# Optimization experiments

Measured on AMD Instinct MI355X. Metric: run time of the kernel, lower is better.

## Reference

```python
import jax, jax.numpy as jnp
import numpy as np

B, S, E, H = 2, 2048, 2048, 16
D = E // H  # head_dim = 128


def _rope_tables(seq_len, dim):
    # standard RoPE: theta_i = 10000^(-2i/dim), angles duplicated over pair halves
    inv_freq = 1.0 / (10000.0 ** (np.arange(0, dim, 2, dtype=np.float32) / dim))
    angles = np.arange(seq_len, dtype=np.float32)[:, None] * inv_freq[None, :]  # [S, D/2]
    angles = np.concatenate([angles, angles], axis=-1)  # [S, D]
    return jnp.asarray(np.cos(angles)), jnp.asarray(np.sin(angles))


def setup_inputs() -> dict:
    key = jax.random.key(0)
    ks = jax.random.split(key, 10)
    sc = 1.0 / np.sqrt(E)
    cos, sin = _rope_tables(S, D)
    mask = jnp.tril(jnp.ones((S, S), dtype=bool))[None, None]  # causal [1,1,S,S]
    return {
        "x_q": jax.random.normal(ks[0], (B, S, E), jnp.float32),
        "x_kv": jax.random.normal(ks[1], (B, S, E), jnp.float32),
        "cos": cos,
        "sin": sin,
        "wq": jax.random.normal(ks[2], (E, E), jnp.float32) * sc,
        "bq": jax.random.normal(ks[3], (E,), jnp.float32) * 0.01,
        "wk": jax.random.normal(ks[4], (E, E), jnp.float32) * sc,
        "bk": jax.random.normal(ks[5], (E,), jnp.float32) * 0.01,
        "wv": jax.random.normal(ks[6], (E, E), jnp.float32) * sc,
        "bv": jax.random.normal(ks[7], (E,), jnp.float32) * 0.01,
        "wo": jax.random.normal(ks[8], (E, E), jnp.float32) * sc,
        "bo": jax.random.normal(ks[9], (E,), jnp.float32) * 0.01,
        "mask": mask,
    }


def _apply_rope(x, cos, sin):
    # x: [B,H,S,D]; cos/sin: [S,D]. rotate-half convention.
    x1, x2 = jnp.split(x, 2, axis=-1)
    rot = jnp.concatenate([-x2, x1], axis=-1)
    return x * cos[None, None] + rot * sin[None, None]


def reference(x_q, x_kv, cos, sin, wq, bq, wk, bk, wv, bv, wo, bo, mask):
    b, sq, _ = x_q.shape
    skv = x_kv.shape[1]
    q = (x_q @ wq.T + bq).reshape(b, sq, H, D).transpose(0, 2, 1, 3)   # [B,H,Sq,D]
    k = (x_kv @ wk.T + bk).reshape(b, skv, H, D).transpose(0, 2, 1, 3)
    v = (x_kv @ wv.T + bv).reshape(b, skv, H, D).transpose(0, 2, 1, 3)
    q = _apply_rope(q, cos, sin)
    k = _apply_rope(k, cos, sin)
    scores = jnp.einsum("bhqd,bhkd->bhqk", q, k) / jnp.sqrt(jnp.float32(D))
    scores = jnp.where(mask, scores, jnp.float32(-1e9))
    w = jax.nn.softmax(scores, axis=-1)  # dropout p=0 -> identity
    out = jnp.einsum("bhqk,bhkd->bhqd", w, v)
    out = out.transpose(0, 2, 1, 3).reshape(b, sq, H * D)
    return out @ wo.T + bo
```

## Files before the change

### kernel.cpp

```cpp
#include <hip/hip_runtime.h>
#include <hip/hip_bf16.h>

#define Bb 2
#define Ss 2048
#define Ee 2048
#define Hh 16
#define Dd 128
#define Mrows (Bb*Ss)

typedef short short8 __attribute__((ext_vector_type(8)));
typedef float f32x4 __attribute__((ext_vector_type(4)));

__device__ __forceinline__ unsigned short bf_rne(float f) {
    unsigned u = __builtin_bit_cast(unsigned, f);
    u += 0x7fffu + ((u >> 16) & 1u);
    return (unsigned short)(u >> 16);
}
__device__ __forceinline__ float bf2f(unsigned short x) {
    unsigned u = ((unsigned)x) << 16;
    return __builtin_bit_cast(float, u);
}
__device__ __forceinline__ void load_lds16(const void* g, void* l) {
    __builtin_amdgcn_global_load_lds(
        (const __attribute__((address_space(1))) unsigned int*)g,
        (__attribute__((address_space(3))) unsigned int*)l, 16, 0, 0);
}

__global__ void cast4_kernel(const float4* __restrict__ in, ushort4* __restrict__ out, int n4) {
    int i = blockIdx.x * 256 + threadIdx.x;
    if (i < n4) {
        float4 v = in[i];
        ushort4 o;
        o.x = bf_rne(v.x); o.y = bf_rne(v.y); o.z = bf_rne(v.z); o.w = bf_rne(v.w);
        out[i] = o;
    }
}

__global__ __launch_bounds__(256) void gemm_bt(
    const short* __restrict__ A, const short* __restrict__ W,
    const float* __restrict__ bias, float* __restrict__ Cf, short* __restrict__ Cb,
    int M, int N, int K, int mode)
{
    __shared__ short As[128*32];
    __shared__ short Bs[128*32];
    const int tid  = threadIdx.x;
    const int wave = tid >> 6;
    const int lane = tid & 63;
    const int quad = lane >> 4;
    const int l16  = lane & 15;
    const int m0 = blockIdx.x * 128;
    const int n0 = blockIdx.y * 128;
    const int wm = (wave & 1) * 64;
    const int wn = (wave >> 1) * 64;

    f32x4 acc[4][4] = {};

    const int srow = wave * 32 + (lane >> 2);
    const int scol = (lane & 3) * 8;
    const size_t a_base = (size_t)(m0 + srow) * K + scol;
    const size_t b_base = (size_t)(n0 + srow) * K + scol;

    for (int kt = 0; kt < K; kt += 32) {
        __syncthreads();
        load_lds16(A + a_base + kt,                 &As[(wave*32) * 32]);
        load_lds16(A + a_base + (size_t)16*K + kt,  &As[(wave*32 + 16) * 32]);
        load_lds16(W + b_base + kt,                 &Bs[(wave*32) * 32]);
        load_lds16(W + b_base + (size_t)16*K + kt,  &Bs[(wave*32 + 16) * 32]);
        __syncthreads();

        short8 af[4], bfr[4];
        #pragma unroll
        for (int i = 0; i < 4; ++i)
            af[i] = *(const short8*)&As[(wm + i*16 + l16)*32 + quad*8];
        #pragma unroll
        for (int j = 0; j < 4; ++j)
            bfr[j] = *(const short8*)&Bs[(wn + j*16 + l16)*32 + quad*8];
        #pragma unroll
        for (int i = 0; i < 4; ++i)
            #pragma unroll
            for (int j = 0; j < 4; ++j)
                acc[i][j] = __builtin_amdgcn_mfma_f32_16x16x32_bf16(af[i], bfr[j], acc[i][j], 0, 0, 0);
    }

    #pragma unroll
    for (int i = 0; i < 4; ++i) {
        #pragma unroll
        for (int j = 0; j < 4; ++j) {
            #pragma unroll
            for (int r = 0; r < 4; ++r) {
                int gm = m0 + wm + i*16 + quad*4 + r;
                int gn = n0 + wn + j*16 + l16;
                if (mode == 0) {
                    Cf[(size_t)gm * N + gn] = acc[i][j][r] + bias[gn];
                } else if (mode == 1) {
                    float v = acc[i][j][r] + bias[gn];
                    int b = gm >> 11, s = gm & (Ss-1);
                    int h = gn >> 7,  d = gn & (Dd-1);
                    Cb[(((size_t)(b*Hh + h)) * Ss + s) * Dd + d] = (short)bf_rne(v);
                } else {
                    float v = acc[i][j][r] + bias[gm];
                    int h = gm >> 7,  d = gm & (Dd-1);
                    int b = gn >> 11, s = gn & (Ss-1);
                    Cb[(((size_t)(b*Hh + h)) * Dd + d) * Ss + s] = (short)bf_rne(v);
                }
            }
        }
    }
}

__global__ void rope_kernel(short* __restrict__ X, const float* __restrict__ cosT,
                            const float* __restrict__ sinT, float scale) {
    int idx = blockIdx.x * 256 + threadIdx.x;
    int d  = idx & 63;
    int s  = (idx >> 6) & (Ss - 1);
    int bh = idx >> 17;
    size_t base = ((size_t)bh * Ss + s) * Dd;
    float x1 = bf2f((unsigned short)X[base + d]);
    float x2 = bf2f((unsigned short)X[base + d + 64]);
    float c  = cosT[s*Dd + d];
    float sn = sinT[s*Dd + d];
    float y1 = (x1 * c - x2 * sn) * scale;
    float y2 = (x2 * c + x1 * sn) * scale;
    X[base + d]      = (short)bf_rne(y1);
    X[base + d + 64] = (short)bf_rne(y2);
}

__global__ __launch_bounds__(256, 2) void attn_kernel(
    const short* __restrict__ Q, const short* __restrict__ Kk,
    const short* __restrict__ VT, short* __restrict__ O)
{
    __shared__ short Ks[64*128];
    __shared__ short Vt[2][128*64];
    __shared__ short Pw[4][32*72];

    const int tid  = threadIdx.x;
    const int wave = tid >> 6;
    const int lane = tid & 63;
    const int quad = lane >> 4;
    const int l16  = lane & 15;
    const int mmap = (blockIdx.x + blockIdx.y) & 15;
    const int qt   = (blockIdx.y & 16) ? (15 - mmap) : mmap;
    const int bh = blockIdx.y;
    const int b  = bh >> 4, h = bh & 15;
    const size_t head_off = (size_t)bh * Ss * Dd;
    const short* Kg  = Kk + head_off;
    const short* VTg = VT + head_off;

    auto stageK = [&](int kt) {
        #pragma unroll
        for (int j = 0; j < 4; ++j) {
            int r = wave*16 + j*4 + (lane >> 4);
            int c = (lane & 15) ^ (r & 15);
            load_lds16(Kg + (size_t)(kt*64 + r)*Dd + c*8, &Ks[(wave*16 + j*4)*128]);
        }
    };
    auto stageV = [&](int kt, int buf) {
        #pragma unroll
        for (int j = 0; j < 4; ++j) {
            int r = wave*32 + j*8 + (lane >> 3);
            int c = (lane & 7) ^ (r & 7);
            load_lds16(VTg + (size_t)r*Ss + kt*64 + c*8, &Vt[buf][(wave*32 + j*8)*64]);
        }
    };

    const int qbase = qt*128 + wave*32;
    short8 qf[2][4];
    #pragma unroll
    for (int mi = 0; mi < 2; ++mi)
        #pragma unroll
        for (int ds = 0; ds < 4; ++ds)
            qf[mi][ds] = *(const short8*)&Q[head_off + (size_t)(qbase + mi*16 + l16)*Dd + ds*32 + quad*8];

    f32x4 o[2][8] = {};
    float m_i[2][4], l_i[2][4];
    #pragma unroll
    for (int mi = 0; mi < 2; ++mi)
        #pragma unroll
        for (int r = 0; r < 4; ++r) { m_i[mi][r] = -__builtin_inff(); l_i[mi][r] = 0.f; }

    const int ktiles = 2*qt + 2;
    stageK(0);
    stageV(0, 0);

    for (int kt = 0; kt < ktiles; ++kt) {
        __syncthreads();
        if (kt + 1 < ktiles) stageV(kt+1, (kt+1)&1);

        f32x4 sc[2][4] = {};
        #pragma unroll
        for (int jk = 0; jk < 4; ++jk)
            #pragma unroll
            for (int ds = 0; ds < 4; ++ds) {
                short8 kf = *(const short8*)&Ks[(jk*16 + l16)*128 + (((ds*4 + quad) ^ l16) * 8)];
                #pragma unroll
                for (int mi = 0; mi < 2; ++mi)
                    sc[mi][jk] = __builtin_amdgcn_mfma_f32_16x16x32_bf16(qf[mi][ds], kf, sc[mi][jk], 0, 0, 0);
            }

        __syncthreads();
        if (kt + 1 < ktiles) stageK(kt+1);

        const int k0 = kt*64;
        #pragma unroll
        for (int mi = 0; mi < 2; ++mi) {
            if (k0 + 63 > qbase + mi*16) {
                #pragma unroll
                for (int jk = 0; jk < 4; ++jk) {
                    int kg = k0 + jk*16 + l16;
                    #pragma unroll
                    for (int r = 0; r < 4; ++r)
                        if (kg > qbase + mi*16 + quad*4 + r) sc[mi][jk][r] = -__builtin_inff();
                }
            }
        }

        float alpha[2][4];
        #pragma unroll
        for (int mi = 0; mi < 2; ++mi)
            #pragma unroll
            for (int r = 0; r < 4; ++r) {
                float mx = fmaxf(fmaxf(sc[mi][0][r], sc[mi][1][r]), fmaxf(sc[mi][2][r], sc[mi][3][r]));
                #pragma unroll
                for (int off = 1; off < 16; off <<= 1)
                    mx = fmaxf(mx, __shfl_xor(mx, off));
                float mn = fmaxf(m_i[mi][r], mx);
                alpha[mi][r] = __expf(m_i[mi][r] - mn);
                m_i[mi][r] = mn;
                float s = 0.f;
                #pragma unroll
                for (int jk = 0; jk < 4; ++jk) {
                    float p = __expf(sc[mi][jk][r] - mn);
                    sc[mi][jk][r] = p;
                    s += p;
                }
                l_i[mi][r] = l_i[mi][r] * alpha[mi][r] + s;
            }

        #pragma unroll
        for (int mi = 0; mi < 2; ++mi)
            #pragma unroll
            for (int jk = 0; jk < 4; ++jk)
                #pragma unroll
                for (int r = 0; r < 4; ++r)
                    Pw[wave][(mi*16 + quad*4 + r)*72 + jk*16 + l16] = (short)bf_rne(sc[mi][jk][r]);

        #pragma unroll
        for (int mi = 0; mi < 2; ++mi)
            #pragma unroll
            for (int dt = 0; dt < 8; ++dt)
                #pragma unroll
                for (int r = 0; r < 4; ++r)
                    o[mi][dt][r] *= alpha[mi][r];

        short8 pa[2][2];
        #pragma unroll
        for (int mi = 0; mi < 2; ++mi)
            #pragma unroll
            for (int kk = 0; kk < 2; ++kk)
                pa[mi][kk] = *(const short8*)&Pw[wave][(mi*16 + l16)*72 + kk*32 + quad*8];

        const short* vb = Vt[kt & 1];
        #pragma unroll
        for (int dt = 0; dt < 8; ++dt)
            #pragma unroll
            for (int kk = 0; kk < 2; ++kk) {
                short8 vf = *(const short8*)&vb[(dt*16 + l16)*64 + (((kk*4 + quad) ^ (l16 & 7)) * 8)];
                #pragma unroll
                for (int mi = 0; mi < 2; ++mi)
                    o[mi][dt] = __builtin_amdgcn_mfma_f32_16x16x32_bf16(pa[mi][kk], vf, o[mi][dt], 0, 0, 0);
            }
    }

    #pragma unroll
    for (int mi = 0; mi < 2; ++mi)
        #pragma unroll
        for (int r = 0; r < 4; ++r) {
            float l = l_i[mi][r];
            #pragma unroll
            for (int off = 1; off < 16; off <<= 1)
                l += __shfl_xor(l, off);
            float inv = 1.0f / l;
            int srow = qbase + mi*16 + quad*4 + r;
            size_t obase = ((size_t)b * Ss + srow) * Ee + h * Dd;
            #pragma unroll
            for (int dt = 0; dt < 8; ++dt)
                O[obase + dt*16 + l16] = (short)bf_rne(o[mi][dt][r] * inv);
        }
}

extern "C" void kernel_launch(void* const* d_in, const int* in_sizes, int n_in,
                              void* d_out, int out_size, void* d_ws, size_t ws_size,
                              hipStream_t stream) {
    const float* x_q  = (const float*)d_in[0];
    const float* x_kv = (const float*)d_in[1];
    const float* cosT = (const float*)d_in[2];
    const float* sinT = (const float*)d_in[3];
    const float* wq = (const float*)d_in[4];
    const float* bq = (const float*)d_in[5];
    const float* wk = (const float*)d_in[6];
    const float* bk = (const float*)d_in[7];
    const float* wv = (const float*)d_in[8];
    const float* bv = (const float*)d_in[9];
    const float* wo = (const float*)d_in[10];
    const float* bo = (const float*)d_in[11];

    size_t off = 0;
    auto alloc = [&](size_t bytes) {
        void* p = (char*)d_ws + off;
        off += (bytes + 255) & ~(size_t)255;
        return p;
    };
    const size_t nX = (size_t)Mrows * Ee;
    const size_t nW = (size_t)Ee * Ee;
    short* xq16  = (short*)alloc(nX * 2);
    short* xkv16 = (short*)alloc(nX * 2);
    short* wq16  = (short*)alloc(nW * 2);
    short* wk16  = (short*)alloc(nW * 2);
    short* wv16  = (short*)alloc(nW * 2);
    short* wo16  = (short*)alloc(nW * 2);
    short* Qr    = (short*)alloc(nX * 2);
    short* Kr    = (short*)alloc(nX * 2);
    short* VTb   = (short*)alloc(nX * 2);
    short* Ob    = (short*)alloc(nX * 2);

    cast4_kernel<<<(int)(nX/4 + 255)/256, 256, 0, stream>>>((const float4*)x_q,  (ushort4*)xq16,  (int)(nX/4));
    cast4_kernel<<<(int)(nX/4 + 255)/256, 256, 0, stream>>>((const float4*)x_kv, (ushort4*)xkv16, (int)(nX/4));
    cast4_kernel<<<(int)(nW/4 + 255)/256, 256, 0, stream>>>((const float4*)wq, (ushort4*)wq16, (int)(nW/4));
    cast4_kernel<<<(int)(nW/4 + 255)/256, 256, 0, stream>>>((const float4*)wk, (ushort4*)wk16, (int)(nW/4));
    cast4_kernel<<<(int)(nW/4 + 255)/256, 256, 0, stream>>>((const float4*)wv, (ushort4*)wv16, (int)(nW/4));
    cast4_kernel<<<(int)(nW/4 + 255)/256, 256, 0, stream>>>((const float4*)wo, (ushort4*)wo16, (int)(nW/4));

    dim3 ggrid(Mrows/128, Ee/128);
    gemm_bt<<<ggrid, 256, 0, stream>>>(xq16,  wq16, bq, nullptr, Qr, Mrows, Ee, Ee, 1);
    gemm_bt<<<ggrid, 256, 0, stream>>>(xkv16, wk16, bk, nullptr, Kr, Mrows, Ee, Ee, 1);
    gemm_bt<<<dim3(Ee/128, Mrows/128), 256, 0, stream>>>(wv16, xkv16, bv, nullptr, VTb, Ee, Mrows, Ee, 2);

    int rope_blocks = (Bb*Hh*Ss*64) / 256;
    rope_kernel<<<rope_blocks, 256, 0, stream>>>(Qr, cosT, sinT, 0.08838834764831845f);
    rope_kernel<<<rope_blocks, 256, 0, stream>>>(Kr, cosT, sinT, 1.0f);

    attn_kernel<<<dim3(16, Bb*Hh), 256, 0, stream>>>(Qr, Kr, VTb, Ob);

    gemm_bt<<<ggrid, 256, 0, stream>>>(Ob, wo16, bo, (float*)d_out, nullptr, Mrows, Ee, Ee, 0);
}
```

Baseline: 543.7 us.

## Merge launches, deepen GEMM K-tile with swizzled LDS, transpose V via shared memory

Folds the six cast launches into one kernel, the Q/K/V projections into one grouped GEMM launch, and the two RoPE launches into one. The GEMM core now loads 64-wide K tiles with an XOR-swizzled LDS layout to avoid bank conflicts and halve the barrier count. The V projection is computed in normal orientation and transposed through a padded shared-memory tile, giving coalesced 16-byte stores to the transposed layout. The cast kernel relies on the workspace buffers being contiguous, and the larger LDS tile may reduce occupancy.

```diff
diff --git a/kernel.cpp b/kernel.cpp
--- a/kernel.cpp
+++ b/kernel.cpp
@@ -26,23 +26,146 @@
         (__attribute__((address_space(3))) unsigned int*)l, 16, 0, 0);
 }
 
-__global__ void cast4_kernel(const float4* __restrict__ in, ushort4* __restrict__ out, int n4) {
+__global__ void cast_all_kernel(const float4* __restrict__ xq, const float4* __restrict__ xkv,
+                                const float4* __restrict__ wq, const float4* __restrict__ wk,
+                                const float4* __restrict__ wv, const float4* __restrict__ wo,
+                                ushort4* __restrict__ out) {
     int i = blockIdx.x * 256 + threadIdx.x;
-    if (i < n4) {
-        float4 v = in[i];
-        ushort4 o;
-        o.x = bf_rne(v.x); o.y = bf_rne(v.y); o.z = bf_rne(v.z); o.w = bf_rne(v.w);
-        out[i] = o;
+    const float4* src;
+    int rel;
+    if (i < 2097152)       { src = xq;  rel = i; }
+    else if (i < 4194304)  { src = xkv; rel = i - 2097152; }
+    else if (i < 5242880)  { src = wq;  rel = i - 4194304; }
+    else if (i < 6291456)  { src = wk;  rel = i - 5242880; }
+    else if (i < 7340032)  { src = wv;  rel = i - 6291456; }
+    else                   { src = wo;  rel = i - 7340032; }
+    float4 v = src[rel];
+    ushort4 o;
+    o.x = bf_rne(v.x); o.y = bf_rne(v.y); o.z = bf_rne(v.z); o.w = bf_rne(v.w);
+    out[i] = o;
+}
+
+__device__ __forceinline__ void gemm_core(
+    const short* __restrict__ A, const short* __restrict__ W, int K,
+    int m0, int n0, int wave, int lane, short* As, short* Bs, f32x4 acc[4][4])
+{
+    const int wm = (wave & 1) * 64;
+    const int wn = (wave >> 1) * 64;
+    const int quad = lane >> 4;
+    const int l16  = lane & 15;
+    const int lrow   = lane >> 3;
+    const int gchunk = (lane & 7) ^ lrow;
+
+    for (int kt = 0; kt < K; kt += 64) {
+        __syncthreads();
+        #pragma unroll
+        for (int j = 0; j < 4; ++j) {
+            int row = wave*32 + j*8 + lrow;
+            load_lds16(A + (size_t)(m0 + row)*K + kt + gchunk*8, &As[(wave*32 + j*8)*64]);
+            load_lds16(W + (size_t)(n0 + row)*K + kt + gchunk*8, &Bs[(wave*32 + j*8)*64]);
+        }
+        __syncthreads();
+
+        #pragma unroll
+        for (int ks = 0; ks < 64; ks += 32) {
+            const int cs = ks >> 3;
+            short8 af[4], bfr[4];
+            #pragma unroll
+            for (int i = 0; i < 4; ++i)
+                af[i] = *(const short8*)&As[(wm + i*16 + l16)*64 + (((cs + quad) ^ (l16 & 7)) << 3)];
+            #pragma unroll
+            for (int j = 0; j < 4; ++j)
+                bfr[j] = *(const short8*)&Bs[(wn + j*16 + l16)*64 + (((cs + quad) ^ (l16 & 7)) << 3)];
+            #pragma unroll
+            for (int i = 0; i < 4; ++i)
+                #pragma unroll
+                for (int j = 0; j < 4; ++j)
+                    acc[i][j] = __builtin_amdgcn_mfma_f32_16x16x32_bf16(af[i], bfr[j], acc[i][j], 0, 0, 0);
+        }
     }
 }
 
-__global__ __launch_bounds__(256) void gemm_bt(
+union GemmSmem {
+    struct { short As[128*64]; short Bs[128*64]; } st;
+    short T[128*137];
+};
+
+__global__ __launch_bounds__(256) void qkv_gemm(
+    const short* __restrict__ xq, const short* __restrict__ xkv,
+    const short* __restrict__ wq, const short* __restrict__ wk, const short* __restrict__ wv,
+    const float* __restrict__ bq, const float* __restrict__ bk, const float* __restrict__ bv,
+    short* __restrict__ Qr, short* __restrict__ Kr, short* __restrict__ VT)
+{
+    __shared__ GemmSmem sm;
+    const int tid  = threadIdx.x;
+    const int wave = tid >> 6;
+    const int lane = tid & 63;
+    const int quad = lane >> 4;
+    const int l16  = lane & 15;
+    const int m0   = blockIdx.x * 128;
+    const int sub  = blockIdx.y >> 4;
+    const int nb   = blockIdx.y & 15;
+    const int n0   = nb * 128;
+    const int wm = (wave & 1) * 64;
+    const int wn = (wave >> 1) * 64;
+
+    const short* A = (sub == 0) ? xq : xkv;
+    const short* W = (sub == 0) ? wq : (sub == 1) ? wk : wv;
+    const float* bias = (sub == 0) ? bq : (sub == 1) ? bk : bv;
+
+    f32x4 acc[4][4] = {};
+    gemm_core(A, W, Ee, m0, n0, wave, lane, sm.st.As, sm.st.Bs, acc);
+
+    const int b0 = m0 >> 11;
+    const int s0 = m0 & (Ss - 1);
+
+    if (sub < 2) {
+        short* out = (sub == 0) ? Qr : Kr;
+        #pragma unroll
+        for (int i = 0; i < 4; ++i)
+            #pragma unroll
+            for (int j = 0; j < 4; ++j)
+                #pragma unroll
+                for (int r = 0; r < 4; ++r) {
+                    int gm = m0 + wm + i*16 + quad*4 + r;
+                    int gn = n0 + wn + j*16 + l16;
+                    float v = acc[i][j][r] + bias[gn];
+                    int b = gm >> 11, s = gm & (Ss-1);
+                    int h = gn >> 7,  d = gn & (Dd-1);
+                    out[(((size_t)(b*Hh + h)) * Ss + s) * Dd + d] = (short)bf_rne(v);
+                }
+    } else {
+        __syncthreads();
+        #pragma unroll
+        for (int i = 0; i < 4; ++i)
+            #pragma unroll
+            for (int j = 0; j < 4; ++j)
+                #pragma unroll
+                for (int r = 0; r < 4; ++r) {
+                    int ml = wm + i*16 + quad*4 + r;
+                    int nl = wn + j*16 + l16;
+                    sm.T[ml*137 + nl] = (short)bf_rne(acc[i][j][r] + bias[n0 + nl]);
+                }
+        __syncthreads();
+        const int g = tid & 15, dbase = tid >> 4;
+        const int h = nb;
+        #pragma unroll
+        for (int dd = 0; dd < 8; ++dd) {
+            int d = dbase + dd*16;
+            short8 v;
+            #pragma unroll
+            for (int c = 0; c < 8; ++c)
+                v[c] = sm.T[(g*8 + c)*137 + d];
+            *(short8*)&VT[(((size_t)(b0*Hh + h)) * Dd + d) * Ss + s0 + g*8] = v;
+        }
+    }
+}
+
+__global__ __launch_bounds__(256) void oproj_gemm(
     const short* __restrict__ A, const short* __restrict__ W,
-    const float* __restrict__ bias, float* __restrict__ Cf, short* __restrict__ Cb,
-    int M, int N, int K, int mode)
+    const float* __restrict__ bias, float* __restrict__ Cf)
 {
-    __shared__ short As[128*32];
-    __shared__ short Bs[128*32];
+    __shared__ GemmSmem sm;
     const int tid  = threadIdx.x;
     const int wave = tid >> 6;
     const int lane = tid & 63;
@@ -54,62 +177,24 @@
     const int wn = (wave >> 1) * 64;
 
     f32x4 acc[4][4] = {};
-
-    const int srow = wave * 32 + (lane >> 2);
-    const int scol = (lane & 3) * 8;
-    const size_t a_base = (size_t)(m0 + srow) * K + scol;
-    const size_t b_base = (size_t)(n0 + srow) * K + scol;
-
-    for (int kt = 0; kt < K; kt += 32) {
-        __syncthreads();
-        load_lds16(A + a_base + kt,                 &As[(wave*32) * 32]);
-        load_lds16(A + a_base + (size_t)16*K + kt,  &As[(wave*32 + 16) * 32]);
-        load_lds16(W + b_base + kt,                 &Bs[(wave*32) * 32]);
-        load_lds16(W + b_base + (size_t)16*K + kt,  &Bs[(wave*32 + 16) * 32]);
-        __syncthreads();
-
-        short8 af[4], bfr[4];
-        #pragma unroll
-        for (int i = 0; i < 4; ++i)
-            af[i] = *(const short8*)&As[(wm + i*16 + l16)*32 + quad*8];
+    gemm_core(A, W, Ee, m0, n0, wave, lane, sm.st.As, sm.st.Bs, acc);
+
+    #pragma unroll
+    for (int i = 0; i < 4; ++i)
         #pragma unroll
         for (int j = 0; j < 4; ++j)
-            bfr[j] = *(const short8*)&Bs[(wn + j*16 + l16)*32 + quad*8];
-        #pragma unroll
-        for (int i = 0; i < 4; ++i)
-            #pragma unroll
-            for (int j = 0; j < 4; ++j)
-                acc[i][j] = __builtin_amdgcn_mfma_f32_16x16x32_bf16(af[i], bfr[j], acc[i][j], 0, 0, 0);
-    }
-
-    #pragma unroll
-    for (int i = 0; i < 4; ++i) {
-        #pragma unroll
-        for (int j = 0; j < 4; ++j) {
             #pragma unroll
             for (int r = 0; r < 4; ++r) {
                 int gm = m0 + wm + i*16 + quad*4 + r;
                 int gn = n0 + wn + j*16 + l16;
-                if (mode == 0) {
-                    Cf[(size_t)gm * N + gn] = acc[i][j][r] + bias[gn];
-                } else if (mode == 1) {
-                    float v = acc[i][j][r] + bias[gn];
-                    int b = gm >> 11, s = gm & (Ss-1);
-                    int h = gn >> 7,  d = gn & (Dd-1);
-                    Cb[(((size_t)(b*Hh + h)) * Ss + s) * Dd + d] = (short)bf_rne(v);
-                } else {
-                    float v = acc[i][j][r] + bias[gm];
-                    int h = gm >> 7,  d = gm & (Dd-1);
-                    int b = gn >> 11, s = gn & (Ss-1);
-                    Cb[(((size_t)(b*Hh + h)) * Dd + d) * Ss + s] = (short)bf_rne(v);
-                }
+                Cf[(size_t)gm * Ee + gn] = acc[i][j][r] + bias[gn];
             }
-        }
-    }
-}
-
-__global__ void rope_kernel(short* __restrict__ X, const float* __restrict__ cosT,
-                            const float* __restrict__ sinT, float scale) {
+}
+
+__global__ void rope_kernel(short* __restrict__ Qr, short* __restrict__ Kr,
+                            const float* __restrict__ cosT, const float* __restrict__ sinT) {
+    short* X    = blockIdx.y ? Kr : Qr;
+    float scale = blockIdx.y ? 1.0f : 0.08838834764831845f;
     int idx = blockIdx.x * 256 + threadIdx.x;
     int d  = idx & 63;
     int s  = (idx >> 6) & (Ss - 1);
@@ -119,10 +204,8 @@
     float x2 = bf2f((unsigned short)X[base + d + 64]);
     float c  = cosT[s*Dd + d];
     float sn = sinT[s*Dd + d];
-    float y1 = (x1 * c - x2 * sn) * scale;
-    float y2 = (x2 * c + x1 * sn) * scale;
-    X[base + d]      = (short)bf_rne(y1);
-    X[base + d + 64] = (short)bf_rne(y2);
+    X[base + d]      = (short)bf_rne((x1 * c - x2 * sn) * scale);
+    X[base + d + 64] = (short)bf_rne((x2 * c + x1 * sn) * scale);
 }
 
 __global__ __launch_bounds__(256, 2) void attn_kernel(
@@ -323,23 +406,16 @@
     short* VTb   = (short*)alloc(nX * 2);
     short* Ob    = (short*)alloc(nX * 2);
 
-    cast4_kernel<<<(int)(nX/4 + 255)/256, 256, 0, stream>>>((const float4*)x_q,  (ushort4*)xq16,  (int)(nX/4));
-    cast4_kernel<<<(int)(nX/4 + 255)/256, 256, 0, stream>>>((const float4*)x_kv, (ushort4*)xkv16, (int)(nX/4));
-    cast4_kernel<<<(int)(nW/4 + 255)/256, 256, 0, stream>>>((const float4*)wq, (ushort4*)wq16, (int)(nW/4));
-    cast4_kernel<<<(int)(nW/4 + 255)/256, 256, 0, stream>>>((const float4*)wk, (ushort4*)wk16, (int)(nW/4));
-    cast4_kernel<<<(int)(nW/4 + 255)/256, 256, 0, stream>>>((const float4*)wv, (ushort4*)wv16, (int)(nW/4));
-    cast4_kernel<<<(int)(nW/4 + 255)/256, 256, 0, stream>>>((const float4*)wo, (ushort4*)wo16, (int)(nW/4));
-
-    dim3 ggrid(Mrows/128, Ee/128);
-    gemm_bt<<<ggrid, 256, 0, stream>>>(xq16,  wq16, bq, nullptr, Qr, Mrows, Ee, Ee, 1);
-    gemm_bt<<<ggrid, 256, 0, stream>>>(xkv16, wk16, bk, nullptr, Kr, Mrows, Ee, Ee, 1);
-    gemm_bt<<<dim3(Ee/128, Mrows/128), 256, 0, stream>>>(wv16, xkv16, bv, nullptr, VTb, Ee, Mrows, Ee, 2);
-
-    int rope_blocks = (Bb*Hh*Ss*64) / 256;
-    rope_kernel<<<rope_blocks, 256, 0, stream>>>(Qr, cosT, sinT, 0.08838834764831845f);
-    rope_kernel<<<rope_blocks, 256, 0, stream>>>(Kr, cosT, sinT, 1.0f);
+    cast_all_kernel<<<32768, 256, 0, stream>>>(
+        (const float4*)x_q, (const float4*)x_kv, (const float4*)wq,
+        (const float4*)wk, (const float4*)wv, (const float4*)wo, (ushort4*)xq16);
+
+    qkv_gemm<<<dim3(Mrows/128, 48), 256, 0, stream>>>(
+        xq16, xkv16, wq16, wk16, wv16, bq, bk, bv, Qr, Kr, VTb);
+
+    rope_kernel<<<dim3((Bb*Hh*Ss*64)/256, 2), 256, 0, stream>>>(Qr, Kr, cosT, sinT);
 
     attn_kernel<<<dim3(16, Bb*Hh), 256, 0, stream>>>(Qr, Kr, VTb, Ob);
 
-    gemm_bt<<<ggrid, 256, 0, stream>>>(Ob, wo16, bo, (float*)d_out, nullptr, Mrows, Ee, Ee, 0);
-}
+    oproj_gemm<<<dim3(Mrows/128, Ee/128), 256, 0, stream>>>(Ob, wo16, bo, (float*)d_out);
+}
```

After: 458.4 us. 15.7% less time.
